# Optimization experiments

Hardware: AMD Instinct MI355X
Metric: run time of the kernel (lower is better)

Reference implementation:

```python
import jax, jax.numpy as jnp
import numpy as np
from jax import lax

GRID_SIZE = 5
SPLINE_ORDER = 3
N_COEF = GRID_SIZE + SPLINE_ORDER  # 8 b-spline basis functions per input
GRID_LO, GRID_HI = -1.0, 1.0


def _grid():
    h = (GRID_HI - GRID_LO) / GRID_SIZE
    return jnp.arange(-SPLINE_ORDER, GRID_SIZE + SPLINE_ORDER + 1, dtype=jnp.float32) * h + GRID_LO


def _bsplines(x):
    # x: [..., in] -> [..., in, N_COEF] via Cox-de Boor recursion (efficient-kan)
    grid = _grid()
    x = x[..., None]
    bases = ((x >= grid[:-1]) & (x < grid[1:])).astype(x.dtype)
    for j in range(1, SPLINE_ORDER + 1):
        bases = ((x - grid[:-(j + 1)]) / (grid[j:-1] - grid[:-(j + 1)]) * bases[..., :-1]
                 + (grid[j + 1:] - x) / (grid[j + 1:] - grid[1:-j]) * bases[..., 1:])
    return bases


def _kan_linear(x, base_w, spline_w):
    # x: [..., in]; base_w: [out, in]; spline_w: [out, in, N_COEF]
    base = jax.nn.silu(x) @ base_w.T
    b = _bsplines(x).reshape(x.shape[:-1] + (-1,))  # [..., in*N_COEF]
    return base + b @ spline_w.reshape(spline_w.shape[0], -1).T


def _kan_conv(x, base_w, spline_w):
    # x: [B, C, H, W]; 3x3 valid KAN convolution
    patches = lax.conv_general_dilated_patches(x, (3, 3), (1, 1), 'VALID')  # [B, C*9, H-2, W-2]
    p = patches.transpose(0, 2, 3, 1)  # [B, Ho, Wo, C*9]
    out = _kan_linear(p, base_w, spline_w)  # [B, Ho, Wo, out]
    return out.transpose(0, 3, 1, 2)


def _maxpool2(x):
    return lax.reduce_window(x, -jnp.inf, lax.max, (1, 1, 2, 2), (1, 1, 2, 2), 'VALID')


def setup_inputs() -> dict:
    key = jax.random.key(0)
    ks = jax.random.split(key, 12)
    B = 2048
    x = jax.random.uniform(ks[0], (B, 1, 28, 28), dtype=jnp.float32)
    s = 0.1
    return {
        'x': x,
        'bw1': jax.random.normal(ks[1], (5, 9), dtype=jnp.float32) * s,
        'sw1': jax.random.normal(ks[2], (5, 9, N_COEF), dtype=jnp.float32) * s,
        'bw2': jax.random.normal(ks[3], (5, 45), dtype=jnp.float32) * s,
        'sw2': jax.random.normal(ks[4], (5, 45, N_COEF), dtype=jnp.float32) * s,
        'bw3': jax.random.normal(ks[5], (2, 45), dtype=jnp.float32) * s,
        'sw3': jax.random.normal(ks[6], (2, 45, N_COEF), dtype=jnp.float32) * s,
        'w1': jax.random.normal(ks[7], (500, 162), dtype=jnp.float32) * 0.05,
        'b1': jnp.zeros((500,), dtype=jnp.float32),
        'w2': jax.random.normal(ks[8], (10, 500), dtype=jnp.float32) * 0.05,
        'b2': jnp.zeros((10,), dtype=jnp.float32),
    }


def reference(x, bw1, sw1, bw2, sw2, bw3, sw3, w1, b1, w2, b2):
    h = _kan_conv(x, bw1, sw1)       # [B, 5, 26, 26]
    h = _maxpool2(h)                 # [B, 5, 13, 13]
    h = _kan_conv(h, bw2, sw2)       # [B, 5, 11, 11]
    h = _kan_conv(h, bw3, sw3)       # [B, 2, 9, 9]
    h = h.reshape(h.shape[0], -1)    # [B, 162]
    h = jax.nn.relu(h @ w1.T + b1)   # [B, 500]
    return h @ w2.T + b2             # [B, 10]
```

## Files before the change

### kernel.cpp

```cpp
#include <hip/hip_runtime.h>


typedef _Float16 h2 __attribute__((ext_vector_type(2)));

__device__ __forceinline__ h2 u2h(unsigned int u) {
  union { unsigned int x; h2 h; } v; v.x = u; return v.h;
}
__device__ __forceinline__ unsigned short f2h_bits(float x) {
  union { _Float16 h; unsigned short u; } v; v.h = (_Float16)x; return v.u;
}
__device__ __forceinline__ unsigned int pack2h(float a, float b) {
  return (unsigned int)f2h_bits(a) | ((unsigned int)f2h_bits(b) << 16);
}
__device__ __forceinline__ float fdot2(h2 a, h2 b, float c) {
  return __builtin_amdgcn_fdot2(a, b, c, false);
}

__device__ __forceinline__ void featurize_regs(float v, uint4& bs, float& silu) {
  silu = v / (1.0f + __expf(-v));
  bs.x = 0u; bs.y = 0u; bs.z = 0u; bs.w = 0u;
  float u = fmaf(v, 2.5f, 5.5f);
  if (u >= 0.0f && u < 11.0f) {
    float tf = floorf(u);
    float f = u - tf, f2 = f * f, f3 = f2 * f, om = 1.0f - f;
    const float c6 = 1.0f / 6.0f;
    float w0 = om * om * om * c6;
    float w1 = (3.0f * f3 - 6.0f * f2 + 4.0f) * c6;
    float w2 = (-3.0f * f3 + 3.0f * f2 + 3.0f * f + 1.0f) * c6;
    float w3 = f3 * c6;
    unsigned long long w01 =
        (unsigned long long)f2h_bits(w0) |
        ((unsigned long long)f2h_bits(w1) << 16) |
        ((unsigned long long)f2h_bits(w2) << 32) |
        ((unsigned long long)f2h_bits(w3) << 48);
    int t = (int)tf;
    int s = 16 * t - 48;
    unsigned long long lo, hi;
    if (s >= 0) {
      lo = (s < 64) ? (w01 << s) : 0ull;
      hi = (s == 0) ? 0ull : ((s < 64) ? (w01 >> (64 - s)) : (w01 << (s - 64)));
    } else {
      lo = w01 >> (-s);
      hi = 0ull;
    }
    bs.x = (unsigned int)lo; bs.y = (unsigned int)(lo >> 32);
    bs.z = (unsigned int)hi; bs.w = (unsigned int)(hi >> 32);
  }
}

__global__ __launch_bounds__(256) void k_prep(
    const float* __restrict__ bw1, const float* __restrict__ sw1,
    const float* __restrict__ bw2, const float* __restrict__ sw2,
    const float* __restrict__ bw3, const float* __restrict__ sw3,
    const float* __restrict__ w1,
    unsigned int* __restrict__ V1s, float* __restrict__ V1b,
    unsigned int* __restrict__ V2s, float* __restrict__ V2b,
    unsigned int* __restrict__ V3s, float* __restrict__ V3b,
    unsigned int* __restrict__ W1p) {
  int t = blockIdx.x * 256 + threadIdx.x;
  if (t < 180) {
    int p = t & 3, o = (t >> 2) % 5, in = t / 20;
    V1s[t] = pack2h(sw1[(o * 9 + in) * 8 + 2 * p], sw1[(o * 9 + in) * 8 + 2 * p + 1]);
  }
  if (t < 45)  { int o = t % 5, in = t / 5; V1b[t] = bw1[o * 9 + in]; }
  if (t < 900) {
    int p = t & 3, o = (t >> 2) % 5, in = t / 20;
    V2s[t] = pack2h(sw2[(o * 45 + in) * 8 + 2 * p], sw2[(o * 45 + in) * 8 + 2 * p + 1]);
  }
  if (t < 225) { int o = t % 5, in = t / 5; V2b[t] = bw2[o * 45 + in]; }
  if (t < 360) {
    int p = t & 3, o = (t >> 2) & 1, in = t / 8;
    V3s[t] = pack2h(sw3[(o * 45 + in) * 8 + 2 * p], sw3[(o * 45 + in) * 8 + 2 * p + 1]);
  }
  if (t < 90)  { int o = t % 2, in = t / 2; V3b[t] = bw3[o * 45 + in]; }
  if (t < 81 * 512) {
    int kp = t >> 9, o = t & 511;
    W1p[t] = (o < 500) ? pack2h(w1[o * 162 + 2 * kp], w1[o * 162 + 2 * kp + 1]) : 0u;
  }
}

__global__ __launch_bounds__(256) void k_fused(
    const float* __restrict__ x,
    const unsigned int* __restrict__ V1s, const float* __restrict__ V1b,
    const unsigned int* __restrict__ V2s, const float* __restrict__ V2b,
    const unsigned int* __restrict__ V3s, const float* __restrict__ V3b,
    const unsigned int* __restrict__ W1p,
    const float* __restrict__ b1,
    const float* __restrict__ W2, const float* __restrict__ b2,
    float* __restrict__ out) {
  __shared__ uint4 bas[845];
  __shared__ float ext[845];
  float*        basF = (float*)bas;
  unsigned int* extU = (unsigned int*)ext;
  const int b = blockIdx.x;
  const int tid = threadIdx.x;

  for (int l = tid; l < 784; l += 256) {
    uint4 bs; float sl;
    featurize_regs(x[b * 784 + l], bs, sl);
    bas[l] = bs; ext[l] = sl;
  }
  __syncthreads();

  float best[5];
  if (tid < 169) {
    int py = tid / 13, px = tid % 13;
    int r0 = py * 2, c0 = px * 2;
    float wacc[4][5];
    #pragma unroll
    for (int wi = 0; wi < 4; ++wi)
      #pragma unroll
      for (int o = 0; o < 5; ++o) wacc[wi][o] = 0.0f;
    #pragma unroll
    for (int r = 0; r < 4; ++r) {
      uint4 q[4]; float sl[4];
      #pragma unroll
      for (int c = 0; c < 4; ++c) {
        q[c]  = bas[(r0 + r) * 28 + c0 + c];
        sl[c] = ext[(r0 + r) * 28 + c0 + c];
      }
      #pragma unroll
      for (int c = 0; c < 4; ++c) {
        h2 a0 = u2h(q[c].x), a1 = u2h(q[c].y), a2 = u2h(q[c].z), a3 = u2h(q[c].w);
        #pragma unroll
        for (int dy = 0; dy < 2; ++dy) {
          #pragma unroll
          for (int dx = 0; dx < 2; ++dx) {
            int ky = r - dy, kx = c - dx;
            if (ky >= 0 && ky < 3 && kx >= 0 && kx < 3) {
              const unsigned int* wp = V1s + (ky * 3 + kx) * 20;
              const float* bp = V1b + (ky * 3 + kx) * 5;
              #pragma unroll
              for (int o = 0; o < 5; ++o) {
                float acc = wacc[dy * 2 + dx][o];
                acc = fdot2(a0, u2h(wp[o * 4 + 0]), acc);
                acc = fdot2(a1, u2h(wp[o * 4 + 1]), acc);
                acc = fdot2(a2, u2h(wp[o * 4 + 2]), acc);
                acc = fdot2(a3, u2h(wp[o * 4 + 3]), acc);
                wacc[dy * 2 + dx][o] = fmaf(sl[c], bp[o], acc);
              }
            }
          }
        }
      }
    }
    #pragma unroll
    for (int o = 0; o < 5; ++o)
      best[o] = fmaxf(fmaxf(wacc[0][o], wacc[1][o]), fmaxf(wacc[2][o], wacc[3][o]));
  }
  __syncthreads();
  if (tid < 169) {
    #pragma unroll
    for (int o = 0; o < 5; ++o) ext[o * 169 + tid] = best[o];
  }
  __syncthreads();

  {
    float hv[4];
    #pragma unroll
    for (int i = 0; i < 4; ++i) {
      int l = tid + i * 256;
      hv[i] = (l < 845) ? ext[l] : 0.0f;
    }
    __syncthreads();
    #pragma unroll
    for (int i = 0; i < 4; ++i) {
      int l = tid + i * 256;
      if (l < 845) {
        uint4 bs; float sl;
        featurize_regs(hv[i], bs, sl);
        bas[l] = bs; ext[l] = sl;
      }
    }
  }
  __syncthreads();

  float acc2[5];
  if (tid < 121) {
    int y = tid / 11, xx = tid % 11;
    #pragma unroll
    for (int o = 0; o < 5; ++o) acc2[o] = 0.0f;
    #pragma unroll 1
    for (int cky = 0; cky < 15; ++cky) {
      int c = cky / 3, ky = cky % 3;
      int base = c * 169 + (y + ky) * 13 + xx;
      uint4 q0 = bas[base], q1 = bas[base + 1], q2 = bas[base + 2];
      float s0 = ext[base], s1 = ext[base + 1], s2 = ext[base + 2];
      uint4 wq[15]; float wb[15];
      const uint4* wp4 = (const uint4*)(V2s + cky * 60);
      const float* bp  = V2b + cky * 15;
      #pragma unroll
      for (int i = 0; i < 15; ++i) { wq[i] = wp4[i]; wb[i] = bp[i]; }
      #pragma unroll
      for (int kx = 0; kx < 3; ++kx) {
        uint4 q = (kx == 0) ? q0 : ((kx == 1) ? q1 : q2);
        float sl = (kx == 0) ? s0 : ((kx == 1) ? s1 : s2);
        h2 a0 = u2h(q.x), a1 = u2h(q.y), a2 = u2h(q.z), a3 = u2h(q.w);
        #pragma unroll
        for (int o = 0; o < 5; ++o) {
          uint4 w = wq[kx * 5 + o];
          float a = acc2[o];
          a = fdot2(a0, u2h(w.x), a);
          a = fdot2(a1, u2h(w.y), a);
          a = fdot2(a2, u2h(w.z), a);
          a = fdot2(a3, u2h(w.w), a);
          acc2[o] = fmaf(sl, wb[kx * 5 + o], a);
        }
      }
    }
  }
  __syncthreads();
  if (tid < 121) {
    #pragma unroll
    for (int o = 0; o < 5; ++o) ext[o * 121 + tid] = acc2[o];
  }
  __syncthreads();

  {
    float hv[3];
    #pragma unroll
    for (int i = 0; i < 3; ++i) {
      int l = tid + i * 256;
      hv[i] = (l < 605) ? ext[l] : 0.0f;
    }
    __syncthreads();
    #pragma unroll
    for (int i = 0; i < 3; ++i) {
      int l = tid + i * 256;
      if (l < 605) {
        uint4 bs; float sl;
        featurize_regs(hv[i], bs, sl);
        bas[l] = bs; ext[l] = sl;
      }
    }
  }
  __syncthreads();

  float acc3[2];
  if (tid < 81) {
    int y = tid / 9, xx = tid % 9;
    acc3[0] = 0.0f; acc3[1] = 0.0f;
    #pragma unroll 1
    for (int cky = 0; cky < 15; ++cky) {
      int c = cky / 3, ky = cky % 3;
      int base = c * 121 + (y + ky) * 11 + xx;
      uint4 q0 = bas[base], q1 = bas[base + 1], q2 = bas[base + 2];
      float s0 = ext[base], s1 = ext[base + 1], s2 = ext[base + 2];
      uint4 wq[6]; float wb[6];
      const uint4* wp4 = (const uint4*)(V3s + cky * 24);
      const float* bp  = V3b + cky * 6;
      #pragma unroll
      for (int i = 0; i < 6; ++i) { wq[i] = wp4[i]; wb[i] = bp[i]; }
      #pragma unroll
      for (int kx = 0; kx < 3; ++kx) {
        uint4 q = (kx == 0) ? q0 : ((kx == 1) ? q1 : q2);
        float sl = (kx == 0) ? s0 : ((kx == 1) ? s1 : s2);
        h2 a0 = u2h(q.x), a1 = u2h(q.y), a2 = u2h(q.z), a3 = u2h(q.w);
        #pragma unroll
        for (int o = 0; o < 2; ++o) {
          uint4 w = wq[kx * 2 + o];
          float a = acc3[o];
          a = fdot2(a0, u2h(w.x), a);
          a = fdot2(a1, u2h(w.y), a);
          a = fdot2(a2, u2h(w.z), a);
          a = fdot2(a3, u2h(w.w), a);
          acc3[o] = fmaf(sl, wb[kx * 2 + o], a);
        }
      }
    }
  }
  __syncthreads();
  if (tid < 81) { ext[tid] = acc3[0]; ext[81 + tid] = acc3[1]; }
  __syncthreads();

  if (tid < 81) extU[256 + tid] = pack2h(ext[2 * tid], ext[2 * tid + 1]);
  __syncthreads();

  if (tid < 250) {
    float a0 = 0.0f, a1 = 0.0f;
    #pragma unroll 4
    for (int kp = 0; kp < 81; ++kp) {
      h2 hk = u2h(extU[256 + kp]);
      uint2 wvv = *(const uint2*)(W1p + kp * 512 + 2 * tid);
      a0 = fdot2(hk, u2h(wvv.x), a0);
      a1 = fdot2(hk, u2h(wvv.y), a1);
    }
    int o0 = 2 * tid, o1 = 2 * tid + 1;
    float v0 = a0 + b1[o0], v1 = a1 + b1[o1];
    basF[160 + o0] = v0 > 0.0f ? v0 : 0.0f;
    basF[160 + o1] = v1 > 0.0f ? v1 : 0.0f;
  }
  __syncthreads();

  if (tid < 160) {
    int o = tid >> 4, part = tid & 15;
    float s = 0.0f;
    #pragma unroll
    for (int j = 0; j < 8; ++j) {
      int k = part * 4 + j * 64;
      if (k <= 496) {
        float4 w = *(const float4*)&W2[o * 500 + k];
        float4 h = *(const float4*)&basF[160 + k];
        s += w.x * h.x + w.y * h.y + w.z * h.z + w.w * h.w;
      }
    }
    basF[tid] = s;
  }
  __syncthreads();

  if (tid < 10) {
    float s = 0.0f;
    #pragma unroll
    for (int p = 0; p < 16; ++p) s += basF[tid * 16 + p];
    out[b * 10 + tid] = s + b2[tid];
  }
}

extern "C" void kernel_launch(void* const* d_in, const int* in_sizes, int n_in,
                              void* d_out, int out_size, void* d_ws, size_t ws_size,
                              hipStream_t stream) {
  (void)in_sizes; (void)n_in; (void)out_size; (void)ws_size;
  const float* x   = (const float*)d_in[0];
  const float* bw1 = (const float*)d_in[1];
  const float* sw1 = (const float*)d_in[2];
  const float* bw2 = (const float*)d_in[3];
  const float* sw2 = (const float*)d_in[4];
  const float* bw3 = (const float*)d_in[5];
  const float* sw3 = (const float*)d_in[6];
  const float* w1  = (const float*)d_in[7];
  const float* b1  = (const float*)d_in[8];
  const float* w2  = (const float*)d_in[9];
  const float* b2  = (const float*)d_in[10];
  float* out = (float*)d_out;

  char* ws = (char*)d_ws;
  unsigned int* V1s = (unsigned int*)(ws);
  float*        V1b = (float*)(ws + 768);
  unsigned int* V2s = (unsigned int*)(ws + 1024);
  float*        V2b = (float*)(ws + 4672);
  unsigned int* V3s = (unsigned int*)(ws + 5632);
  float*        V3b = (float*)(ws + 7168);
  unsigned int* W1p = (unsigned int*)(ws + 7680);

  k_prep<<<162, 256, 0, stream>>>(bw1, sw1, bw2, sw2, bw3, sw3, w1,
                                  V1s, V1b, V2s, V2b, V3s, V3b, W1p);
  k_fused<<<2048, 256, 0, stream>>>(x, V1s, V1b, V2s, V2b, V3s, V3b, W1p,
                                    b1, w2, b2, out);
}
```

Measured before the change: 139.7 us.

## Run each image on a single wavefront and drop block-level barriers

The fused kernel now runs one 64-lane wavefront per image instead of a 256-thread block. It loops over spatial positions and keeps intermediate activations in registers so all __syncthreads are removed. The FC1 weights are repacked so each lane reads uint4 chunks covering four k-pairs, and FC2 weights are padded to 512 so the final layer can use a wave shuffle reduction. This removes barrier and idle-thread overhead, but each block now has a quarter of the threads doing the same work serially, and 2048 single-wave blocks may leave the GPU underoccupied.

```diff
diff --git a/kernel.cpp b/kernel.cpp
--- a/kernel.cpp
+++ b/kernel.cpp
@@ -52,11 +52,11 @@
     const float* __restrict__ bw1, const float* __restrict__ sw1,
     const float* __restrict__ bw2, const float* __restrict__ sw2,
     const float* __restrict__ bw3, const float* __restrict__ sw3,
-    const float* __restrict__ w1,
+    const float* __restrict__ w1, const float* __restrict__ w2,
     unsigned int* __restrict__ V1s, float* __restrict__ V1b,
     unsigned int* __restrict__ V2s, float* __restrict__ V2b,
     unsigned int* __restrict__ V3s, float* __restrict__ V3b,
-    unsigned int* __restrict__ W1p) {
+    unsigned int* __restrict__ W1p4, float* __restrict__ W2p) {
   int t = blockIdx.x * 256 + threadIdx.x;
   if (t < 180) {
     int p = t & 3, o = (t >> 2) % 5, in = t / 20;
@@ -73,246 +73,261 @@
     V3s[t] = pack2h(sw3[(o * 45 + in) * 8 + 2 * p], sw3[(o * 45 + in) * 8 + 2 * p + 1]);
   }
   if (t < 90)  { int o = t % 2, in = t / 2; V3b[t] = bw3[o * 45 + in]; }
-  if (t < 81 * 512) {
-    int kp = t >> 9, o = t & 511;
-    W1p[t] = (o < 500) ? pack2h(w1[o * 162 + 2 * kp], w1[o * 162 + 2 * kp + 1]) : 0u;
-  }
-}
-
-__global__ __launch_bounds__(256) void k_fused(
+  if (t < 43008) {
+    int j = t & 3, o = (t >> 2) & 511, kpq = t >> 11;
+    int kp = kpq * 4 + j;
+    W1p4[t] = (o < 500 && kp < 81)
+                  ? pack2h(w1[o * 162 + 2 * kp], w1[o * 162 + 2 * kp + 1])
+                  : 0u;
+  }
+  if (t < 5120) {
+    int o = t >> 9, k = t & 511;
+    W2p[t] = (k < 500) ? w2[o * 500 + k] : 0.0f;
+  }
+}
+
+__global__ __launch_bounds__(64, 2) void k_fused(
     const float* __restrict__ x,
     const unsigned int* __restrict__ V1s, const float* __restrict__ V1b,
     const unsigned int* __restrict__ V2s, const float* __restrict__ V2b,
     const unsigned int* __restrict__ V3s, const float* __restrict__ V3b,
-    const unsigned int* __restrict__ W1p,
-    const float* __restrict__ b1,
-    const float* __restrict__ W2, const float* __restrict__ b2,
+    const unsigned int* __restrict__ W1p4, const float* __restrict__ W2p,
+    const float* __restrict__ b1, const float* __restrict__ b2,
     float* __restrict__ out) {
   __shared__ uint4 bas[845];
-  __shared__ float ext[845];
+  __shared__ float slu[845];
   float*        basF = (float*)bas;
-  unsigned int* extU = (unsigned int*)ext;
+  unsigned int* hpk  = (unsigned int*)slu + 256;
   const int b = blockIdx.x;
-  const int tid = threadIdx.x;
-
-  for (int l = tid; l < 784; l += 256) {
+  const int lane = threadIdx.x;
+
+  for (int l = lane; l < 784; l += 64) {
     uint4 bs; float sl;
     featurize_regs(x[b * 784 + l], bs, sl);
-    bas[l] = bs; ext[l] = sl;
-  }
-  __syncthreads();
-
-  float best[5];
-  if (tid < 169) {
-    int py = tid / 13, px = tid % 13;
-    int r0 = py * 2, c0 = px * 2;
-    float wacc[4][5];
-    #pragma unroll
-    for (int wi = 0; wi < 4; ++wi)
-      #pragma unroll
-      for (int o = 0; o < 5; ++o) wacc[wi][o] = 0.0f;
-    #pragma unroll
-    for (int r = 0; r < 4; ++r) {
-      uint4 q[4]; float sl[4];
-      #pragma unroll
-      for (int c = 0; c < 4; ++c) {
-        q[c]  = bas[(r0 + r) * 28 + c0 + c];
-        sl[c] = ext[(r0 + r) * 28 + c0 + c];
-      }
-      #pragma unroll
-      for (int c = 0; c < 4; ++c) {
-        h2 a0 = u2h(q[c].x), a1 = u2h(q[c].y), a2 = u2h(q[c].z), a3 = u2h(q[c].w);
-        #pragma unroll
-        for (int dy = 0; dy < 2; ++dy) {
+    bas[l] = bs; slu[l] = sl;
+  }
+
+  float h1v[3][5];
+  #pragma unroll 1
+  for (int it = 0; it < 3; ++it) {
+    int p = it * 64 + lane;
+    if (p < 169) {
+      int py = p / 13, px = p % 13;
+      int r0 = py * 2, c0 = px * 2;
+      float wacc[4][5];
+      #pragma unroll
+      for (int wi = 0; wi < 4; ++wi)
+        #pragma unroll
+        for (int o = 0; o < 5; ++o) wacc[wi][o] = 0.0f;
+      #pragma unroll
+      for (int r = 0; r < 4; ++r) {
+        uint4 q[4]; float sl[4];
+        #pragma unroll
+        for (int c = 0; c < 4; ++c) {
+          q[c]  = bas[(r0 + r) * 28 + c0 + c];
+          sl[c] = slu[(r0 + r) * 28 + c0 + c];
+        }
+        #pragma unroll
+        for (int c = 0; c < 4; ++c) {
+          h2 a0 = u2h(q[c].x), a1 = u2h(q[c].y), a2 = u2h(q[c].z), a3 = u2h(q[c].w);
           #pragma unroll
-          for (int dx = 0; dx < 2; ++dx) {
-            int ky = r - dy, kx = c - dx;
-            if (ky >= 0 && ky < 3 && kx >= 0 && kx < 3) {
-              const unsigned int* wp = V1s + (ky * 3 + kx) * 20;
-              const float* bp = V1b + (ky * 3 + kx) * 5;
-              #pragma unroll
-              for (int o = 0; o < 5; ++o) {
-                float acc = wacc[dy * 2 + dx][o];
-                acc = fdot2(a0, u2h(wp[o * 4 + 0]), acc);
-                acc = fdot2(a1, u2h(wp[o * 4 + 1]), acc);
-                acc = fdot2(a2, u2h(wp[o * 4 + 2]), acc);
-                acc = fdot2(a3, u2h(wp[o * 4 + 3]), acc);
-                wacc[dy * 2 + dx][o] = fmaf(sl[c], bp[o], acc);
+          for (int dy = 0; dy < 2; ++dy) {
+            #pragma unroll
+            for (int dx = 0; dx < 2; ++dx) {
+              int ky = r - dy, kx = c - dx;
+              if (ky >= 0 && ky < 3 && kx >= 0 && kx < 3) {
+                const unsigned int* wp = V1s + (ky * 3 + kx) * 20;
+                const float* bp = V1b + (ky * 3 + kx) * 5;
+                #pragma unroll
+                for (int o = 0; o < 5; ++o) {
+                  float acc = wacc[dy * 2 + dx][o];
+                  acc = fdot2(a0, u2h(wp[o * 4 + 0]), acc);
+                  acc = fdot2(a1, u2h(wp[o * 4 + 1]), acc);
+                  acc = fdot2(a2, u2h(wp[o * 4 + 2]), acc);
+                  acc = fdot2(a3, u2h(wp[o * 4 + 3]), acc);
+                  wacc[dy * 2 + dx][o] = fmaf(sl[c], bp[o], acc);
+                }
               }
             }
           }
         }
       }
-    }
+      #pragma unroll
+      for (int o = 0; o < 5; ++o)
+        h1v[it][o] = fmaxf(fmaxf(wacc[0][o], wacc[1][o]),
+                           fmaxf(wacc[2][o], wacc[3][o]));
+    }
+  }
+  #pragma unroll 1
+  for (int it = 0; it < 3; ++it) {
+    int p = it * 64 + lane;
+    if (p < 169) {
+      #pragma unroll
+      for (int o = 0; o < 5; ++o) {
+        uint4 bs; float sl;
+        featurize_regs(h1v[it][o], bs, sl);
+        bas[o * 169 + p] = bs; slu[o * 169 + p] = sl;
+      }
+    }
+  }
+
+  float h2v[2][5];
+  #pragma unroll 1
+  for (int it = 0; it < 2; ++it) {
+    int pos = it * 64 + lane;
+    if (pos < 121) {
+      int y = pos / 11, xx = pos % 11;
+      float acc2[5];
+      #pragma unroll
+      for (int o = 0; o < 5; ++o) acc2[o] = 0.0f;
+      #pragma unroll 1
+      for (int cky = 0; cky < 15; ++cky) {
+        int c = cky / 3, ky = cky % 3;
+        int base = c * 169 + (y + ky) * 13 + xx;
+        uint4 q0 = bas[base], q1 = bas[base + 1], q2 = bas[base + 2];
+        float s0 = slu[base], s1 = slu[base + 1], s2 = slu[base + 2];
+        uint4 wq[15]; float wb[15];
+        const uint4* wp4 = (const uint4*)(V2s + cky * 60);
+        const float* bp  = V2b + cky * 15;
+        #pragma unroll
+        for (int i = 0; i < 15; ++i) { wq[i] = wp4[i]; wb[i] = bp[i]; }
+        #pragma unroll
+        for (int kx = 0; kx < 3; ++kx) {
+          uint4 q = (kx == 0) ? q0 : ((kx == 1) ? q1 : q2);
+          float sl = (kx == 0) ? s0 : ((kx == 1) ? s1 : s2);
+          h2 a0 = u2h(q.x), a1 = u2h(q.y), a2 = u2h(q.z), a3 = u2h(q.w);
+          #pragma unroll
+          for (int o = 0; o < 5; ++o) {
+            uint4 w = wq[kx * 5 + o];
+            float a = acc2[o];
+            a = fdot2(a0, u2h(w.x), a);
+            a = fdot2(a1, u2h(w.y), a);
+            a = fdot2(a2, u2h(w.z), a);
+            a = fdot2(a3, u2h(w.w), a);
+            acc2[o] = fmaf(sl, wb[kx * 5 + o], a);
+          }
+        }
+      }
+      #pragma unroll
+      for (int o = 0; o < 5; ++o) h2v[it][o] = acc2[o];
+    }
+  }
+  #pragma unroll 1
+  for (int it = 0; it < 2; ++it) {
+    int pos = it * 64 + lane;
+    if (pos < 121) {
+      #pragma unroll
+      for (int o = 0; o < 5; ++o) {
+        uint4 bs; float sl;
+        featurize_regs(h2v[it][o], bs, sl);
+        bas[o * 121 + pos] = bs; slu[o * 121 + pos] = sl;
+      }
+    }
+  }
+
+  float h3v[2][2];
+  #pragma unroll 1
+  for (int it = 0; it < 2; ++it) {
+    int pos = it * 64 + lane;
+    if (pos < 81) {
+      int y = pos / 9, xx = pos % 9;
+      float acc3[2] = {0.f, 0.f};
+      #pragma unroll 1
+      for (int cky = 0; cky < 15; ++cky) {
+        int c = cky / 3, ky = cky % 3;
+        int base = c * 121 + (y + ky) * 11 + xx;
+        uint4 q0 = bas[base], q1 = bas[base + 1], q2 = bas[base + 2];
+        float s0 = slu[base], s1 = slu[base + 1], s2 = slu[base + 2];
+        uint4 wq[6]; float wb[6];
+        const uint4* wp4 = (const uint4*)(V3s + cky * 24);
+        const float* bp  = V3b + cky * 6;
+        #pragma unroll
+        for (int i = 0; i < 6; ++i) { wq[i] = wp4[i]; wb[i] = bp[i]; }
+        #pragma unroll
+        for (int kx = 0; kx < 3; ++kx) {
+          uint4 q = (kx == 0) ? q0 : ((kx == 1) ? q1 : q2);
+          float sl = (kx == 0) ? s0 : ((kx == 1) ? s1 : s2);
+          h2 a0 = u2h(q.x), a1 = u2h(q.y), a2 = u2h(q.z), a3 = u2h(q.w);
+          #pragma unroll
+          for (int o = 0; o < 2; ++o) {
+            uint4 w = wq[kx * 2 + o];
+            float a = acc3[o];
+            a = fdot2(a0, u2h(w.x), a);
+            a = fdot2(a1, u2h(w.y), a);
+            a = fdot2(a2, u2h(w.z), a);
+            a = fdot2(a3, u2h(w.w), a);
+            acc3[o] = fmaf(sl, wb[kx * 2 + o], a);
+          }
+        }
+      }
+      h3v[it][0] = acc3[0]; h3v[it][1] = acc3[1];
+    }
+  }
+  #pragma unroll 1
+  for (int it = 0; it < 2; ++it) {
+    int pos = it * 64 + lane;
+    if (pos < 81) { slu[pos] = h3v[it][0]; slu[81 + pos] = h3v[it][1]; }
+  }
+  hpk[lane] = pack2h(slu[2 * lane], slu[2 * lane + 1]);
+  {
+    int i1 = 64 + lane;
+    if (i1 < 84)
+      hpk[i1] = (i1 < 81) ? pack2h(slu[2 * i1], slu[2 * i1 + 1]) : 0u;
+  }
+
+  float fa[8];
+  #pragma unroll
+  for (int i = 0; i < 8; ++i) fa[i] = 0.0f;
+  {
+    const uint4* hp4 = (const uint4*)hpk;
+    #pragma unroll 1
+    for (int kpq = 0; kpq < 21; ++kpq) {
+      uint4 hk = hp4[kpq];
+      const uint4* wrow = (const uint4*)W1p4 + kpq * 512 + lane;
+      #pragma unroll
+      for (int i = 0; i < 8; ++i) {
+        uint4 wv = wrow[i * 64];
+        float a = fa[i];
+        a = fdot2(u2h(hk.x), u2h(wv.x), a);
+        a = fdot2(u2h(hk.y), u2h(wv.y), a);
+        a = fdot2(u2h(hk.z), u2h(wv.z), a);
+        a = fdot2(u2h(hk.w), u2h(wv.w), a);
+        fa[i] = a;
+      }
+    }
+  }
+  #pragma unroll
+  for (int i = 0; i < 8; ++i) {
+    int o = lane + 64 * i;
+    float bb = (o < 500) ? b1[o] : 0.0f;
+    float v = fa[i] + bb;
+    basF[o] = (v > 0.0f && o < 500) ? v : 0.0f;
+  }
+
+  float hv0, hv1, hv2, hv3, hv4, hv5, hv6, hv7;
+  {
+    const float4* hf = (const float4*)&basF[lane * 8];
+    float4 ha = hf[0], hb = hf[1];
+    hv0 = ha.x; hv1 = ha.y; hv2 = ha.z; hv3 = ha.w;
+    hv4 = hb.x; hv5 = hb.y; hv6 = hb.z; hv7 = hb.w;
+  }
+  float acc10[10];
+  #pragma unroll
+  for (int o = 0; o < 10; ++o) {
+    const float4* wp = (const float4*)&W2p[o * 512 + lane * 8];
+    float4 w0 = wp[0], w1v = wp[1];
+    float s = hv0 * w0.x + hv1 * w0.y + hv2 * w0.z + hv3 * w0.w;
+    s += hv4 * w1v.x + hv5 * w1v.y + hv6 * w1v.z + hv7 * w1v.w;
+    acc10[o] = s;
+  }
+  #pragma unroll
+  for (int off = 32; off > 0; off >>= 1) {
     #pragma unroll
-    for (int o = 0; o < 5; ++o)
-      best[o] = fmaxf(fmaxf(wacc[0][o], wacc[1][o]), fmaxf(wacc[2][o], wacc[3][o]));
-  }
-  __syncthreads();
-  if (tid < 169) {
+    for (int o = 0; o < 10; ++o) acc10[o] += __shfl_down(acc10[o], off);
+  }
+  if (lane == 0) {
     #pragma unroll
-    for (int o = 0; o < 5; ++o) ext[o * 169 + tid] = best[o];
-  }
-  __syncthreads();
-
-  {
-    float hv[4];
-    #pragma unroll
-    for (int i = 0; i < 4; ++i) {
-      int l = tid + i * 256;
-      hv[i] = (l < 845) ? ext[l] : 0.0f;
-    }
-    __syncthreads();
-    #pragma unroll
-    for (int i = 0; i < 4; ++i) {
-      int l = tid + i * 256;
-      if (l < 845) {
-        uint4 bs; float sl;
-        featurize_regs(hv[i], bs, sl);
-        bas[l] = bs; ext[l] = sl;
-      }
-    }
-  }
-  __syncthreads();
-
-  float acc2[5];
-  if (tid < 121) {
-    int y = tid / 11, xx = tid % 11;
-    #pragma unroll
-    for (int o = 0; o < 5; ++o) acc2[o] = 0.0f;
-    #pragma unroll 1
-    for (int cky = 0; cky < 15; ++cky) {
-      int c = cky / 3, ky = cky % 3;
-      int base = c * 169 + (y + ky) * 13 + xx;
-      uint4 q0 = bas[base], q1 = bas[base + 1], q2 = bas[base + 2];
-      float s0 = ext[base], s1 = ext[base + 1], s2 = ext[base + 2];
-      uint4 wq[15]; float wb[15];
-      const uint4* wp4 = (const uint4*)(V2s + cky * 60);
-      const float* bp  = V2b + cky * 15;
-      #pragma unroll
-      for (int i = 0; i < 15; ++i) { wq[i] = wp4[i]; wb[i] = bp[i]; }
-      #pragma unroll
-      for (int kx = 0; kx < 3; ++kx) {
-        uint4 q = (kx == 0) ? q0 : ((kx == 1) ? q1 : q2);
-        float sl = (kx == 0) ? s0 : ((kx == 1) ? s1 : s2);
-        h2 a0 = u2h(q.x), a1 = u2h(q.y), a2 = u2h(q.z), a3 = u2h(q.w);
-        #pragma unroll
-        for (int o = 0; o < 5; ++o) {
-          uint4 w = wq[kx * 5 + o];
-          float a = acc2[o];
-          a = fdot2(a0, u2h(w.x), a);
-          a = fdot2(a1, u2h(w.y), a);
-          a = fdot2(a2, u2h(w.z), a);
-          a = fdot2(a3, u2h(w.w), a);
-          acc2[o] = fmaf(sl, wb[kx * 5 + o], a);
-        }
-      }
-    }
-  }
-  __syncthreads();
-  if (tid < 121) {
-    #pragma unroll
-    for (int o = 0; o < 5; ++o) ext[o * 121 + tid] = acc2[o];
-  }
-  __syncthreads();
-
-  {
-    float hv[3];
-    #pragma unroll
-    for (int i = 0; i < 3; ++i) {
-      int l = tid + i * 256;
-      hv[i] = (l < 605) ? ext[l] : 0.0f;
-    }
-    __syncthreads();
-    #pragma unroll
-    for (int i = 0; i < 3; ++i) {
-      int l = tid + i * 256;
-      if (l < 605) {
-        uint4 bs; float sl;
-        featurize_regs(hv[i], bs, sl);
-        bas[l] = bs; ext[l] = sl;
-      }
-    }
-  }
-  __syncthreads();
-
-  float acc3[2];
-  if (tid < 81) {
-    int y = tid / 9, xx = tid % 9;
-    acc3[0] = 0.0f; acc3[1] = 0.0f;
-    #pragma unroll 1
-    for (int cky = 0; cky < 15; ++cky) {
-      int c = cky / 3, ky = cky % 3;
-      int base = c * 121 + (y + ky) * 11 + xx;
-      uint4 q0 = bas[base], q1 = bas[base + 1], q2 = bas[base + 2];
-      float s0 = ext[base], s1 = ext[base + 1], s2 = ext[base + 2];
-      uint4 wq[6]; float wb[6];
-      const uint4* wp4 = (const uint4*)(V3s + cky * 24);
-      const float* bp  = V3b + cky * 6;
-      #pragma unroll
-      for (int i = 0; i < 6; ++i) { wq[i] = wp4[i]; wb[i] = bp[i]; }
-      #pragma unroll
-      for (int kx = 0; kx < 3; ++kx) {
-        uint4 q = (kx == 0) ? q0 : ((kx == 1) ? q1 : q2);
-        float sl = (kx == 0) ? s0 : ((kx == 1) ? s1 : s2);
-        h2 a0 = u2h(q.x), a1 = u2h(q.y), a2 = u2h(q.z), a3 = u2h(q.w);
-        #pragma unroll
-        for (int o = 0; o < 2; ++o) {
-          uint4 w = wq[kx * 2 + o];
-          float a = acc3[o];
-          a = fdot2(a0, u2h(w.x), a);
-          a = fdot2(a1, u2h(w.y), a);
-          a = fdot2(a2, u2h(w.z), a);
-          a = fdot2(a3, u2h(w.w), a);
-          acc3[o] = fmaf(sl, wb[kx * 2 + o], a);
-        }
-      }
-    }
-  }
-  __syncthreads();
-  if (tid < 81) { ext[tid] = acc3[0]; ext[81 + tid] = acc3[1]; }
-  __syncthreads();
-
-  if (tid < 81) extU[256 + tid] = pack2h(ext[2 * tid], ext[2 * tid + 1]);
-  __syncthreads();
-
-  if (tid < 250) {
-    float a0 = 0.0f, a1 = 0.0f;
-    #pragma unroll 4
-    for (int kp = 0; kp < 81; ++kp) {
-      h2 hk = u2h(extU[256 + kp]);
-      uint2 wvv = *(const uint2*)(W1p + kp * 512 + 2 * tid);
-      a0 = fdot2(hk, u2h(wvv.x), a0);
-      a1 = fdot2(hk, u2h(wvv.y), a1);
-    }
-    int o0 = 2 * tid, o1 = 2 * tid + 1;
-    float v0 = a0 + b1[o0], v1 = a1 + b1[o1];
-    basF[160 + o0] = v0 > 0.0f ? v0 : 0.0f;
-    basF[160 + o1] = v1 > 0.0f ? v1 : 0.0f;
-  }
-  __syncthreads();
-
-  if (tid < 160) {
-    int o = tid >> 4, part = tid & 15;
-    float s = 0.0f;
-    #pragma unroll
-    for (int j = 0; j < 8; ++j) {
-      int k = part * 4 + j * 64;
-      if (k <= 496) {
-        float4 w = *(const float4*)&W2[o * 500 + k];
-        float4 h = *(const float4*)&basF[160 + k];
-        s += w.x * h.x + w.y * h.y + w.z * h.z + w.w * h.w;
-      }
-    }
-    basF[tid] = s;
-  }
-  __syncthreads();
-
-  if (tid < 10) {
-    float s = 0.0f;
-    #pragma unroll
-    for (int p = 0; p < 16; ++p) s += basF[tid * 16 + p];
-    out[b * 10 + tid] = s + b2[tid];
+    for (int o = 0; o < 10; ++o) out[b * 10 + o] = acc10[o] + b2[o];
   }
 }
 
@@ -334,16 +349,17 @@
   float* out = (float*)d_out;
 
   char* ws = (char*)d_ws;
-  unsigned int* V1s = (unsigned int*)(ws);
-  float*        V1b = (float*)(ws + 768);
-  unsigned int* V2s = (unsigned int*)(ws + 1024);
-  float*        V2b = (float*)(ws + 4672);
-  unsigned int* V3s = (unsigned int*)(ws + 5632);
-  float*        V3b = (float*)(ws + 7168);
-  unsigned int* W1p = (unsigned int*)(ws + 7680);
-
-  k_prep<<<162, 256, 0, stream>>>(bw1, sw1, bw2, sw2, bw3, sw3, w1,
-                                  V1s, V1b, V2s, V2b, V3s, V3b, W1p);
-  k_fused<<<2048, 256, 0, stream>>>(x, V1s, V1b, V2s, V2b, V3s, V3b, W1p,
-                                    b1, w2, b2, out);
-}
+  unsigned int* V1s  = (unsigned int*)(ws);
+  float*        V1b  = (float*)(ws + 768);
+  unsigned int* V2s  = (unsigned int*)(ws + 1024);
+  float*        V2b  = (float*)(ws + 4672);
+  unsigned int* V3s  = (unsigned int*)(ws + 5632);
+  float*        V3b  = (float*)(ws + 7168);
+  float*        W2p  = (float*)(ws + 7680);
+  unsigned int* W1p4 = (unsigned int*)(ws + 28672);
+
+  k_prep<<<168, 256, 0, stream>>>(bw1, sw1, bw2, sw2, bw3, sw3, w1, w2,
+                                  V1s, V1b, V2s, V2b, V3s, V3b, W1p4, W2p);
+  k_fused<<<2048, 64, 0, stream>>>(x, V1s, V1b, V2s, V2b, V3s, V3b,
+                                   W1p4, W2p, b1, b2, out);
+}
```

Measured after the change: 136.8 us. 2.0% less time.
